# Kernel optimization log

Measured on AMD Instinct MI355X. Metric: run time of the kernel, lower is better.

The kernel has to match this reference:

```python
import jax, jax.numpy as jnp
import numpy as np

B, T, C, H = 4, 2048, 1024, 16
HD = C // H  # head dim = 64


def setup_inputs() -> dict:
    key = jax.random.key(0)
    k1, k2, k3, k4, k5 = jax.random.split(key, 5)
    s_in = 1.0 / np.sqrt(C)
    return {
        "x": jax.random.normal(k1, (B, T, C), dtype=jnp.float32),
        "W_attn": jax.random.uniform(k2, (C, 3 * C), dtype=jnp.float32, minval=-s_in, maxval=s_in),
        "b_attn": jax.random.uniform(k3, (3 * C,), dtype=jnp.float32, minval=-s_in, maxval=s_in),
        "W_proj": jax.random.uniform(k4, (C, C), dtype=jnp.float32, minval=-s_in, maxval=s_in),
        "b_proj": jax.random.uniform(k5, (C,), dtype=jnp.float32, minval=-s_in, maxval=s_in),
    }


def reference(x, W_attn, b_attn, W_proj, b_proj):
    Bx, Tx, Cx = x.shape
    qkv = x @ W_attn + b_attn                      # [B,T,3C]
    q, k, v = jnp.split(qkv, 3, axis=2)
    # [B,T,C] -> [B,H,T,HD]
    def heads(t):
        return t.reshape(Bx, Tx, H, HD).transpose(0, 2, 1, 3)
    q, k, v = heads(q), heads(k), heads(v)
    scale = 1.0 / np.sqrt(HD).astype(np.float32)
    att = jnp.einsum('bhqd,bhkd->bhqk', q, k) * scale
    causal = jnp.tril(jnp.ones((Tx, Tx), dtype=bool))
    att = jnp.where(causal[None, None], att, -jnp.inf)
    att = jax.nn.softmax(att, axis=-1)
    y = jnp.einsum('bhqk,bhkd->bhqd', att, v)      # [B,H,T,HD]
    y = y.transpose(0, 2, 1, 3).reshape(Bx, Tx, Cx)
    return y @ W_proj + b_proj
```

## Files before the change

kernel.cpp:

```cpp
#include <hip/hip_runtime.h>
#include <math.h>

#define Bn 4
#define Tn 2048
#define Cn 1024
#define Hn 16
#define HDn 64
#define Mn (Bn * Tn)

typedef unsigned short u16;
typedef unsigned int u32;
typedef __attribute__((ext_vector_type(8))) short bf16x8;
typedef __attribute__((ext_vector_type(8))) unsigned short us8;
typedef __attribute__((ext_vector_type(4))) float f32x4;
typedef __attribute__((ext_vector_type(16))) float f32x16;
typedef __attribute__((ext_vector_type(4))) unsigned int u32x4;

__device__ __forceinline__ float b2f(u16 u) {
    return __uint_as_float(((u32)u) << 16);
}
__device__ __forceinline__ u16 f2b(float f) {
    u32 u = __float_as_uint(f);
    return (u16)((u + 0x7FFFu + ((u >> 16) & 1u)) >> 16);
}
__device__ __forceinline__ u32 cvtpk(float a, float b) {
    u32 d;
    asm("v_cvt_pk_bf16_f32 %0, %1, %2" : "=v"(d) : "v"(a), "v"(b));
    return d;
}
__device__ __forceinline__ void pswap(u32& a, u32& b) {
    asm("v_permlane32_swap_b32 %0, %1" : "+v"(a), "+v"(b));
}
__device__ __forceinline__ float max3f(float a, float b, float c) {
    float d;
    asm("v_max3_f32 %0, %1, %2, %3" : "=v"(d) : "v"(a), "v"(b), "v"(c));
    return d;
}
#define EXP2R(x) __builtin_amdgcn_exp2f(x)

__device__ __forceinline__ int xcd_work(int bid, int nwg) {
    return (bid & 7) * (nwg >> 3) + (bid >> 3);
}

#define GLL(srcp, dstp)                                                     \
    __builtin_amdgcn_global_load_lds(                                       \
        (const __attribute__((address_space(1))) u32*)(srcp),               \
        (__attribute__((address_space(3))) u32*)(dstp), 16, 0, 0)

#define WAITCNT6() asm volatile("s_waitcnt vmcnt(6)" ::: "memory")
#define WAITCNT4() asm volatile("s_waitcnt vmcnt(4)" ::: "memory")
#define WAITCNT0() asm volatile("s_waitcnt vmcnt(0)" ::: "memory")

__global__ __launch_bounds__(256) void cvt_f32_bf16_kernel(
    const float4* __restrict__ in, ushort4* __restrict__ out, int n4)
{
    for (int i = blockIdx.x * 256 + threadIdx.x; i < n4; i += gridDim.x * 256) {
        float4 v = in[i];
        ushort4 o;
        o.x = f2b(v.x); o.y = f2b(v.y); o.z = f2b(v.z); o.w = f2b(v.w);
        out[i] = o;
    }
}

__global__ __launch_bounds__(256) void transpose_cvt_kernel(
    const float* __restrict__ in, u16* __restrict__ out, int R, int Cc)
{
    __shared__ u16 t[32][33];
    const int c0 = blockIdx.x * 32, r0 = blockIdx.y * 32;
    const int tx = threadIdx.x & 31, ty = threadIdx.x >> 5;
    #pragma unroll
    for (int i = 0; i < 32; i += 8)
        t[ty + i][tx] = f2b(in[(size_t)(r0 + ty + i) * Cc + c0 + tx]);
    __syncthreads();
    #pragma unroll
    for (int i = 0; i < 32; i += 8)
        out[(size_t)(c0 + ty + i) * R + r0 + tx] = t[tx][ty + i];
}

__global__ __launch_bounds__(256, 2) void gemm_qkv_kernel(
    const u16* __restrict__ A, const u16* __restrict__ BT,
    const float* __restrict__ bias,
    u16* __restrict__ outb, u16* __restrict__ vTout,
    int N, int K, int nx)
{
    __shared__ u16 Al[3][128 * 32];
    __shared__ u16 Bl[3][256 * 32];

    const int tid = threadIdx.x;
    const int workid = xcd_work(blockIdx.x, gridDim.x);
    const int brow = (workid / nx) * 128;
    const int bcol = (workid % nx) * 256;
    const int w  = tid >> 6;
    const int wr = w >> 1, wc = w & 1;
    const int l  = tid & 63;
    const int lr = l & 15;
    const int lk = (l >> 4) << 3;

    const int sr = l >> 2;
    const int sc = (l & 3) << 3;

    f32x4 acc[4][8];
    #pragma unroll
    for (int m = 0; m < 4; ++m)
        #pragma unroll
        for (int n = 0; n < 8; ++n) acc[m][n] = (f32x4){0.f, 0.f, 0.f, 0.f};

    #define STAGE_G(k0, bufi)                                                   \
        do {                                                                    \
            GLL(&A [(size_t)(brow + 32 * w +      sr) * K + (k0) + sc],         \
                &Al[bufi][(32 * w) * 32]);                                      \
            GLL(&A [(size_t)(brow + 32 * w + 16 + sr) * K + (k0) + sc],         \
                &Al[bufi][(32 * w + 16) * 32]);                                 \
            GLL(&BT[(size_t)(bcol + 64 * w +      sr) * K + (k0) + sc],         \
                &Bl[bufi][(64 * w) * 32]);                                      \
            GLL(&BT[(size_t)(bcol + 64 * w + 16 + sr) * K + (k0) + sc],         \
                &Bl[bufi][(64 * w + 16) * 32]);                                 \
            GLL(&BT[(size_t)(bcol + 64 * w + 32 + sr) * K + (k0) + sc],         \
                &Bl[bufi][(64 * w + 32) * 32]);                                 \
            GLL(&BT[(size_t)(bcol + 64 * w + 48 + sr) * K + (k0) + sc],         \
                &Bl[bufi][(64 * w + 48) * 32]);                                 \
        } while (0)

    const int T = K >> 5;
    STAGE_G(0, 0);
    STAGE_G(32, 1);

    int cur = 0;
    for (int t = 0; t < T; ++t) {
        if (t < T - 1) WAITCNT6();
        else           WAITCNT0();
        __builtin_amdgcn_s_barrier();

        if (t + 2 < T) {
            const int nb = cur + 2 >= 3 ? cur - 1 : cur + 2;
            STAGE_G((t + 2) << 5, nb);
        }

        bf16x8 a[4], b[8];
        #pragma unroll
        for (int m = 0; m < 4; ++m)
            a[m] = *(const bf16x8*)&Al[cur][(wr * 64 + m * 16 + lr) * 32 + lk];
        #pragma unroll
        for (int n = 0; n < 8; ++n)
            b[n] = *(const bf16x8*)&Bl[cur][(wc * 128 + n * 16 + lr) * 32 + lk];

        __builtin_amdgcn_s_setprio(1);
        #pragma unroll
        for (int m = 0; m < 4; ++m)
            #pragma unroll
            for (int n = 0; n < 8; ++n)
                acc[m][n] = __builtin_amdgcn_mfma_f32_16x16x32_bf16(
                    a[m], b[n], acc[m][n], 0, 0, 0);
        __builtin_amdgcn_s_setprio(0);

        cur = cur == 2 ? 0 : cur + 1;
    }
    #undef STAGE_G

    const int orow0 = brow + wr * 64 + ((l >> 4) << 2);
    const int ocol0 = bcol + wc * 128 + lr;
    if (bcol >= 2048) {
        #pragma unroll
        for (int n = 0; n < 8; ++n) {
            const int c = ocol0 + n * 16 - 2048;
            const float bv = bias[ocol0 + n * 16];
            #pragma unroll
            for (int m = 0; m < 4; ++m) {
                const int row0 = orow0 + m * 16;
                const int bb = row0 >> 11, t0 = row0 & 2047;
                ushort4 pk;
                pk.x = f2b(acc[m][n][0] + bv);
                pk.y = f2b(acc[m][n][1] + bv);
                pk.z = f2b(acc[m][n][2] + bv);
                pk.w = f2b(acc[m][n][3] + bv);
                *(ushort4*)&vTout[((size_t)bb * Cn + c) * Tn + t0] = pk;
            }
        }
    } else {
        #pragma unroll
        for (int n = 0; n < 8; ++n) {
            const int col = ocol0 + n * 16;
            const float bv = bias[col];
            #pragma unroll
            for (int m = 0; m < 4; ++m) {
                #pragma unroll
                for (int r = 0; r < 4; ++r) {
                    const int row = orow0 + m * 16 + r;
                    outb[(size_t)row * N + col] = f2b(acc[m][n][r] + bv);
                }
            }
        }
    }
}

__global__ __launch_bounds__(256) void gemm_proj_kernel(
    const u16* __restrict__ A, const u16* __restrict__ BT,
    const float* __restrict__ bias, float* __restrict__ outf,
    int N, int K, int nx)
{
    __shared__ u16 Al[3][128 * 32];
    __shared__ u16 Bl[3][128 * 32];

    const int tid = threadIdx.x;
    const int workid = xcd_work(blockIdx.x, gridDim.x);
    const int brow = (workid / nx) * 128;
    const int bcol = (workid % nx) * 128;
    const int w  = tid >> 6;
    const int wr = w >> 1, wc = w & 1;
    const int l  = tid & 63;
    const int lr = l & 15;
    const int lk = (l >> 4) << 3;

    const int r0s = tid >> 2,            c0s = (tid & 3) << 3;
    const int r1s = (256 + tid) >> 2;
    const int d0s = (tid & 192) * 8;
    const int d1s = (256 + (tid & 192)) * 8;

    f32x4 acc[4][4];
    #pragma unroll
    for (int m = 0; m < 4; ++m)
        #pragma unroll
        for (int n = 0; n < 4; ++n) acc[m][n] = (f32x4){0.f, 0.f, 0.f, 0.f};

    #define STAGE_P(k0, bufi)                                                \
        do {                                                                 \
            GLL(&A [(size_t)(brow + r0s) * K + (k0) + c0s], &Al[bufi][d0s]); \
            GLL(&BT[(size_t)(bcol + r0s) * K + (k0) + c0s], &Bl[bufi][d0s]); \
            GLL(&A [(size_t)(brow + r1s) * K + (k0) + c0s], &Al[bufi][d1s]); \
            GLL(&BT[(size_t)(bcol + r1s) * K + (k0) + c0s], &Bl[bufi][d1s]); \
        } while (0)

    const int T = K >> 5;
    STAGE_P(0, 0);
    STAGE_P(32, 1);

    int cur = 0;
    for (int t = 0; t < T; ++t) {
        if (t < T - 1) WAITCNT4();
        else           WAITCNT0();
        __builtin_amdgcn_s_barrier();

        if (t + 2 < T) {
            const int nb = cur + 2 >= 3 ? cur - 1 : cur + 2;
            STAGE_P((t + 2) << 5, nb);
        }

        bf16x8 a[4], b[4];
        #pragma unroll
        for (int m = 0; m < 4; ++m)
            a[m] = *(const bf16x8*)&Al[cur][(wr * 64 + m * 16 + lr) * 32 + lk];
        #pragma unroll
        for (int n = 0; n < 4; ++n)
            b[n] = *(const bf16x8*)&Bl[cur][(wc * 64 + n * 16 + lr) * 32 + lk];

        __builtin_amdgcn_s_setprio(1);
        #pragma unroll
        for (int m = 0; m < 4; ++m)
            #pragma unroll
            for (int n = 0; n < 4; ++n)
                acc[m][n] = __builtin_amdgcn_mfma_f32_16x16x32_bf16(
                    a[m], b[n], acc[m][n], 0, 0, 0);
        __builtin_amdgcn_s_setprio(0);

        cur = cur == 2 ? 0 : cur + 1;
    }
    #undef STAGE_P

    const int orow0 = brow + wr * 64 + ((l >> 4) << 2);
    const int ocol0 = bcol + wc * 64 + lr;
    #pragma unroll
    for (int n = 0; n < 4; ++n) {
        const int col = ocol0 + n * 16;
        const float bv = bias[col];
        #pragma unroll
        for (int m = 0; m < 4; ++m) {
            #pragma unroll
            for (int r = 0; r < 4; ++r) {
                const int row = orow0 + m * 16 + r;
                outf[(size_t)row * N + col] = acc[m][n][r] + bv;
            }
        }
    }
}

__global__ __launch_bounds__(256, 2) void attn_mfma8_kernel(
    const u16* __restrict__ qkvb, const u16* __restrict__ vT,
    u16* __restrict__ yb)
{
    __shared__ u16 Kb[3][64 * 64];
    __shared__ u16 Vb[3][64 * 64];

    const int tid = threadIdx.x;
    const int w   = tid >> 6;
    const int l   = tid & 63;
    const int q31 = l & 31;
    const int hi  = l >> 5;
    const int work = xcd_work(blockIdx.x, 512);
    const int pr  = work & 7;
    const int bh  = work >> 3;
    const int b   = bh >> 4, h = bh & 15;

    const float S2 = 0.18033688f;

    const u16* Kg = qkvb + (size_t)(b * Tn) * (3 * Cn) + Cn + h * HDn;
    const u16* Vg = vT + (size_t)bh * HDn * Tn;

    const int srow = l >> 3;
    const int schk = ((l & 7) ^ srow) << 3;
    const int rloc = w * 16;
    const int rsw8 = q31 & 7;

    #define STAGE_A(kt, bufi)                                                  \
        do {                                                                   \
            _Pragma("unroll")                                                  \
            for (int jc = 0; jc < 2; ++jc) {                                   \
                const int rr = rloc + jc * 8;                                  \
                GLL(Kg + (size_t)((kt) * 64 + rr + srow) * (3 * Cn) + schk,    \
                    &Kb[bufi][rr * 64]);                                       \
                GLL(Vg + (size_t)(rr + srow) * Tn + (kt) * 64 + schk,          \
                    &Vb[bufi][rr * 64]);                                       \
            }                                                                  \
        } while (0)

    #pragma unroll 1
    for (int half = 0; half < 2; ++half) {
        const int qt = half ? (15 - pr) : pr;
        const int ktmax = 2 * qt + 2;
        const int qrow0 = qt * 128 + w * 32;
        const int qglob = qrow0 + q31;

        const u16* Qp = qkvb + (size_t)(b * Tn + qglob) * (3 * Cn)
                        + h * HDn + hi * 8;
        bf16x8 qf[4];
        #pragma unroll
        for (int c = 0; c < 4; ++c) qf[c] = *(const bf16x8*)(Qp + c * 16);

        f32x16 O0, O1;
        #pragma unroll
        for (int r = 0; r < 16; ++r) { O0[r] = 0.f; O1[r] = 0.f; }
        float m = -INFINITY, ls = 0.f;

        STAGE_A(0, 0);
        STAGE_A(1, 1);

        int cur = 0;
        for (int kt = 0; kt < ktmax; ++kt) {
            if (kt < ktmax - 1) WAITCNT4();
            else                WAITCNT0();
            __builtin_amdgcn_s_barrier();

            if (kt + 2 < ktmax) {
                const int nb = cur + 2 >= 3 ? cur - 1 : cur + 2;
                STAGE_A(kt + 2, nb);
            }
            const u16* Kc = Kb[cur];
            const u16* Vc = Vb[cur];

            if (kt * 64 <= qrow0 + 31) {
                f32x16 S0, S1;
                #pragma unroll
                for (int r = 0; r < 16; ++r) { S0[r] = 0.f; S1[r] = 0.f; }
                __builtin_amdgcn_s_setprio(1);
                #pragma unroll
                for (int c = 0; c < 4; ++c) {
                    const int co = ((2 * c + hi) ^ rsw8) << 3;
                    const bf16x8 k0 = *(const bf16x8*)&Kc[q31 * 64 + co];
                    const bf16x8 k1 = *(const bf16x8*)&Kc[(32 + q31) * 64 + co];
                    S0 = __builtin_amdgcn_mfma_f32_32x32x16_bf16(k0, qf[c], S0, 0, 0, 0);
                    S1 = __builtin_amdgcn_mfma_f32_32x32x16_bf16(k1, qf[c], S1, 0, 0, 0);
                }
                __builtin_amdgcn_s_setprio(0);

                if (kt * 64 + 63 > qrow0) {
                    #pragma unroll
                    for (int r = 0; r < 16; ++r) {
                        const int kl = kt * 64 + (r & 3) + 8 * (r >> 2) + 4 * hi;
                        if (kl > qglob)      S0[r] = -INFINITY;
                        if (kl + 32 > qglob) S1[r] = -INFINITY;
                    }
                }

                float a0 = max3f(S0[0],  S0[1],  S0[2]);
                float a1 = max3f(S0[3],  S0[4],  S0[5]);
                float a2 = max3f(S0[6],  S0[7],  S0[8]);
                float a3 = max3f(S0[9],  S0[10], S0[11]);
                float a4 = max3f(S0[12], S0[13], S0[14]);
                float a5 = max3f(S0[15], S1[0],  S1[1]);
                float a6 = max3f(S1[2],  S1[3],  S1[4]);
                float a7 = max3f(S1[5],  S1[6],  S1[7]);
                float a8 = max3f(S1[8],  S1[9],  S1[10]);
                float a9 = max3f(S1[11], S1[12], S1[13]);
                float aA = fmaxf(S1[14], S1[15]);
                float b0 = max3f(a0, a1, a2);
                float b1 = max3f(a3, a4, a5);
                float b2 = max3f(a6, a7, a8);
                float b3 = fmaxf(a9, aA);
                float mt = fmaxf(fmaxf(b0, b1), fmaxf(b2, b3));
                mt = fmaxf(mt, __shfl_xor(mt, 32));

                float lscale = 1.f;
                if (__any(mt > m + 64.f)) {
                    const float mn = fmaxf(m, mt);
                    const float alpha = EXP2R((m - mn) * S2);
                    m = mn; lscale = alpha;
                    #pragma unroll
                    for (int r = 0; r < 16; ++r) {
                        const int qloc = (r & 3) + 8 * (r >> 2) + 4 * hi;
                        const float ar = __shfl(alpha, qloc);
                        O0[r] *= ar; O1[r] *= ar;
                    }
                }

                const float nms2 = -m * S2;
                float lt0 = 0.f, lt1 = 0.f;
                u32 w0[8], w1[8];
                #pragma unroll
                for (int i = 0; i < 8; ++i) {
                    const float p0 = EXP2R(fmaf(S0[2 * i],     S2, nms2));
                    const float p1 = EXP2R(fmaf(S0[2 * i + 1], S2, nms2));
                    const float p2 = EXP2R(fmaf(S1[2 * i],     S2, nms2));
                    const float p3 = EXP2R(fmaf(S1[2 * i + 1], S2, nms2));
                    lt0 += (p0 + p1);
                    lt1 += (p2 + p3);
                    w0[i] = cvtpk(p0, p1);
                    w1[i] = cvtpk(p2, p3);
                }
                float lt = lt0 + lt1;
                lt += __shfl_xor(lt, 32);
                ls = ls * lscale + lt;

                __builtin_amdgcn_s_setprio(1);
                #pragma unroll
                for (int t2 = 0; t2 < 2; ++t2) {
                    #pragma unroll
                    for (int c1 = 0; c1 < 2; ++c1) {
                        u32 a0w = t2 ? w1[4 * c1 + 0] : w0[4 * c1 + 0];
                        u32 b0w = t2 ? w1[4 * c1 + 2] : w0[4 * c1 + 2];
                        u32 a1w = t2 ? w1[4 * c1 + 1] : w0[4 * c1 + 1];
                        u32 b1w = t2 ? w1[4 * c1 + 3] : w0[4 * c1 + 3];
                        pswap(a0w, b0w);
                        pswap(a1w, b1w);
                        u32x4 fr; fr.x = a0w; fr.y = a1w; fr.z = b0w; fr.w = b1w;
                        const bf16x8 pf = __builtin_bit_cast(bf16x8, fr);
                        const int c = t2 * 2 + c1;
                        const int co = ((2 * c + hi) ^ rsw8) << 3;
                        const bf16x8 v0 = *(const bf16x8*)&Vc[q31 * 64 + co];
                        const bf16x8 v1 = *(const bf16x8*)&Vc[(32 + q31) * 64 + co];
                        O0 = __builtin_amdgcn_mfma_f32_32x32x16_bf16(pf, v0, O0, 0, 0, 0);
                        O1 = __builtin_amdgcn_mfma_f32_32x32x16_bf16(pf, v1, O1, 0, 0, 0);
                    }
                }
                __builtin_amdgcn_s_setprio(0);
            }

            cur = cur == 2 ? 0 : cur + 1;
        }

        __builtin_amdgcn_s_barrier();

        #pragma unroll
        for (int r = 0; r < 16; ++r) {
            const int qloc = (r & 3) + 8 * (r >> 2) + 4 * hi;
            const float inv = __builtin_amdgcn_rcpf(__shfl(ls, qloc));
            u16* yp = yb + (size_t)(b * Tn + qrow0 + qloc) * Cn + h * HDn + q31;
            yp[0]  = f2b(O0[r] * inv);
            yp[32] = f2b(O1[r] * inv);
        }
    }
    #undef STAGE_A
}

extern "C" void kernel_launch(void* const* d_in, const int* in_sizes, int n_in,
                              void* d_out, int out_size, void* d_ws, size_t ws_size,
                              hipStream_t stream)
{
    const float* x      = (const float*)d_in[0];
    const float* W_attn = (const float*)d_in[1];
    const float* b_attn = (const float*)d_in[2];
    const float* W_proj = (const float*)d_in[3];
    const float* b_proj = (const float*)d_in[4];
    float* out = (float*)d_out;

    u16* xb   = (u16*)d_ws;
    u16* WaT  = xb   + (size_t)Mn * Cn;
    u16* WpT  = WaT  + (size_t)3 * Cn * Cn;
    u16* qkvb = WpT  + (size_t)Cn * Cn;
    u16* yb   = qkvb + (size_t)Mn * 3 * Cn;
    u16* vT   = yb   + (size_t)Mn * Cn;

    cvt_f32_bf16_kernel<<<2048, 256, 0, stream>>>(
        (const float4*)x, (ushort4*)xb, Mn * Cn / 4);

    transpose_cvt_kernel<<<dim3(3 * Cn / 32, Cn / 32), 256, 0, stream>>>(
        W_attn, WaT, Cn, 3 * Cn);
    transpose_cvt_kernel<<<dim3(Cn / 32, Cn / 32), 256, 0, stream>>>(
        W_proj, WpT, Cn, Cn);

    gemm_qkv_kernel<<<64 * 12, 256, 0, stream>>>(
        xb, WaT, b_attn, qkvb, vT, 3 * Cn, Cn, 12);

    attn_mfma8_kernel<<<512, 256, 0, stream>>>(qkvb, vT, yb);

    gemm_proj_kernel<<<8 * 64, 256, 0, stream>>>(
        yb, WpT, b_proj, out, Cn, Cn, 8);
}
```

Before: 178.7 us.

## Restructure QKV GEMM to 256x256 tiles with 8 waves and swizzled LDS

The QKV projection GEMM now uses 256x256 output tiles computed by 512 threads (8 waves in a 2x4 grid), where it used 128x256 tiles with 4 waves. Each k-step is split into two half-phases separated by barriers, with the A and B global-to-LDS loads interleaved between them. An XOR swizzle on the LDS chunk index is meant to reduce bank conflicts on fragment reads. The aim is more operand reuse per tile and better overlap of loads with MFMA work. The cost is higher LDS use, extra barriers per iteration, and only 384 workgroups, which may leave the GPU less evenly loaded.

```diff
diff --git a/kernel.cpp b/kernel.cpp
--- a/kernel.cpp
+++ b/kernel.cpp
@@ -47,9 +47,9 @@
         (const __attribute__((address_space(1))) u32*)(srcp),               \
         (__attribute__((address_space(3))) u32*)(dstp), 16, 0, 0)
 
-#define WAITCNT6() asm volatile("s_waitcnt vmcnt(6)" ::: "memory")
 #define WAITCNT4() asm volatile("s_waitcnt vmcnt(4)" ::: "memory")
 #define WAITCNT0() asm volatile("s_waitcnt vmcnt(0)" ::: "memory")
+#define SCHEDB()   __builtin_amdgcn_sched_barrier(0)
 
 __global__ __launch_bounds__(256) void cvt_f32_bf16_kernel(
     const float4* __restrict__ in, ushort4* __restrict__ out, int n4)
@@ -77,95 +77,114 @@
         out[(size_t)(c0 + ty + i) * R + r0 + tx] = t[tx][ty + i];
 }
 
-__global__ __launch_bounds__(256, 2) void gemm_qkv_kernel(
+__global__ __launch_bounds__(512, 2) void gemm_qkv8_kernel(
     const u16* __restrict__ A, const u16* __restrict__ BT,
     const float* __restrict__ bias,
     u16* __restrict__ outb, u16* __restrict__ vTout,
     int N, int K, int nx)
 {
-    __shared__ u16 Al[3][128 * 32];
+    __shared__ u16 Al[3][256 * 32];
     __shared__ u16 Bl[3][256 * 32];
 
     const int tid = threadIdx.x;
     const int workid = xcd_work(blockIdx.x, gridDim.x);
-    const int brow = (workid / nx) * 128;
+    const int brow = (workid / nx) * 256;
     const int bcol = (workid % nx) * 256;
     const int w  = tid >> 6;
-    const int wr = w >> 1, wc = w & 1;
+    const int wm = w >> 2, wn = w & 3;
     const int l  = tid & 63;
     const int lr = l & 15;
-    const int lk = (l >> 4) << 3;
-
-    const int sr = l >> 2;
-    const int sc = (l & 3) << 3;
-
-    f32x4 acc[4][8];
+    const int g  = l >> 4;
+    const int rk = ((g ^ ((lr >> 1) & 3)) << 3);
+
+    const int srow = l >> 2;
+    const int schk = ((l & 3) ^ ((l >> 3) & 3)) << 3;
+
+    f32x4 acc[8][4];
     #pragma unroll
-    for (int m = 0; m < 4; ++m)
-        #pragma unroll
-        for (int n = 0; n < 8; ++n) acc[m][n] = (f32x4){0.f, 0.f, 0.f, 0.f};
-
-    #define STAGE_G(k0, bufi)                                                   \
-        do {                                                                    \
-            GLL(&A [(size_t)(brow + 32 * w +      sr) * K + (k0) + sc],         \
-                &Al[bufi][(32 * w) * 32]);                                      \
-            GLL(&A [(size_t)(brow + 32 * w + 16 + sr) * K + (k0) + sc],         \
-                &Al[bufi][(32 * w + 16) * 32]);                                 \
-            GLL(&BT[(size_t)(bcol + 64 * w +      sr) * K + (k0) + sc],         \
-                &Bl[bufi][(64 * w) * 32]);                                      \
-            GLL(&BT[(size_t)(bcol + 64 * w + 16 + sr) * K + (k0) + sc],         \
-                &Bl[bufi][(64 * w + 16) * 32]);                                 \
-            GLL(&BT[(size_t)(bcol + 64 * w + 32 + sr) * K + (k0) + sc],         \
-                &Bl[bufi][(64 * w + 32) * 32]);                                 \
-            GLL(&BT[(size_t)(bcol + 64 * w + 48 + sr) * K + (k0) + sc],         \
-                &Bl[bufi][(64 * w + 48) * 32]);                                 \
+    for (int m = 0; m < 8; ++m)
+        #pragma unroll
+        for (int n = 0; n < 4; ++n) acc[m][n] = (f32x4){0.f, 0.f, 0.f, 0.f};
+
+    #define STG_A(k0, bufi)                                                    \
+        do {                                                                   \
+            GLL(&A[(size_t)(brow +       w * 16 + srow) * K + (k0) + schk],    \
+                &Al[bufi][(w * 16) * 32]);                                     \
+            GLL(&A[(size_t)(brow + 128 + w * 16 + srow) * K + (k0) + schk],    \
+                &Al[bufi][(128 + w * 16) * 32]);                               \
         } while (0)
+    #define STG_B(k0, bufi)                                                    \
+        do {                                                                   \
+            GLL(&BT[(size_t)(bcol +       w * 16 + srow) * K + (k0) + schk],   \
+                &Bl[bufi][(w * 16) * 32]);                                     \
+            GLL(&BT[(size_t)(bcol + 128 + w * 16 + srow) * K + (k0) + schk],   \
+                &Bl[bufi][(128 + w * 16) * 32]);                               \
+        } while (0)
 
     const int T = K >> 5;
-    STAGE_G(0, 0);
-    STAGE_G(32, 1);
-
-    int cur = 0;
+    STG_A(0, 0);  STG_B(0, 0);
+    STG_A(32, 1); STG_B(32, 1);
+
     for (int t = 0; t < T; ++t) {
-        if (t < T - 1) WAITCNT6();
+        const int cur = t % 3;
+        const int nxt = (t + 2) % 3;
+        const int k0n = (t + 2) << 5;
+        const u16* Ac = Al[cur];
+        const u16* Bc = Bl[cur];
+
+        if (t < T - 1) WAITCNT4();
         else           WAITCNT0();
         __builtin_amdgcn_s_barrier();
-
-        if (t + 2 < T) {
-            const int nb = cur + 2 >= 3 ? cur - 1 : cur + 2;
-            STAGE_G((t + 2) << 5, nb);
-        }
-
-        bf16x8 a[4], b[8];
+        SCHEDB();
+        if (t + 2 < T) STG_A(k0n, nxt);
+
+        bf16x8 bfr[4], afr[4];
+        #pragma unroll
+        for (int n = 0; n < 4; ++n)
+            bfr[n] = *(const bf16x8*)&Bc[(wn * 64 + n * 16 + lr) * 32 + rk];
         #pragma unroll
         for (int m = 0; m < 4; ++m)
-            a[m] = *(const bf16x8*)&Al[cur][(wr * 64 + m * 16 + lr) * 32 + lk];
-        #pragma unroll
-        for (int n = 0; n < 8; ++n)
-            b[n] = *(const bf16x8*)&Bl[cur][(wc * 128 + n * 16 + lr) * 32 + lk];
+            afr[m] = *(const bf16x8*)&Ac[(wm * 128 + m * 16 + lr) * 32 + rk];
 
         __builtin_amdgcn_s_setprio(1);
         #pragma unroll
         for (int m = 0; m < 4; ++m)
             #pragma unroll
-            for (int n = 0; n < 8; ++n)
+            for (int n = 0; n < 4; ++n)
                 acc[m][n] = __builtin_amdgcn_mfma_f32_16x16x32_bf16(
-                    a[m], b[n], acc[m][n], 0, 0, 0);
+                    afr[m], bfr[n], acc[m][n], 0, 0, 0);
         __builtin_amdgcn_s_setprio(0);
-
-        cur = cur == 2 ? 0 : cur + 1;
+        __builtin_amdgcn_s_barrier();
+        SCHEDB();
+
+        if (t + 2 < T) STG_B(k0n, nxt);
+        #pragma unroll
+        for (int m = 0; m < 4; ++m)
+            afr[m] = *(const bf16x8*)&Ac[(wm * 128 + 64 + m * 16 + lr) * 32 + rk];
+
+        __builtin_amdgcn_s_setprio(1);
+        #pragma unroll
+        for (int m = 0; m < 4; ++m)
+            #pragma unroll
+            for (int n = 0; n < 4; ++n)
+                acc[4 + m][n] = __builtin_amdgcn_mfma_f32_16x16x32_bf16(
+                    afr[m], bfr[n], acc[4 + m][n], 0, 0, 0);
+        __builtin_amdgcn_s_setprio(0);
+        __builtin_amdgcn_s_barrier();
+        SCHEDB();
     }
-    #undef STAGE_G
-
-    const int orow0 = brow + wr * 64 + ((l >> 4) << 2);
-    const int ocol0 = bcol + wc * 128 + lr;
+    #undef STG_A
+    #undef STG_B
+
+    const int orow0 = brow + wm * 128 + (g << 2);
+    const int ocol0 = bcol + wn * 64 + lr;
     if (bcol >= 2048) {
         #pragma unroll
-        for (int n = 0; n < 8; ++n) {
+        for (int n = 0; n < 4; ++n) {
             const int c = ocol0 + n * 16 - 2048;
             const float bv = bias[ocol0 + n * 16];
             #pragma unroll
-            for (int m = 0; m < 4; ++m) {
+            for (int m = 0; m < 8; ++m) {
                 const int row0 = orow0 + m * 16;
                 const int bb = row0 >> 11, t0 = row0 & 2047;
                 ushort4 pk;
@@ -178,11 +197,11 @@
         }
     } else {
         #pragma unroll
-        for (int n = 0; n < 8; ++n) {
+        for (int n = 0; n < 4; ++n) {
             const int col = ocol0 + n * 16;
             const float bv = bias[col];
             #pragma unroll
-            for (int m = 0; m < 4; ++m) {
+            for (int m = 0; m < 8; ++m) {
                 #pragma unroll
                 for (int r = 0; r < 4; ++r) {
                     const int row = orow0 + m * 16 + r;
@@ -496,7 +515,7 @@
     transpose_cvt_kernel<<<dim3(Cn / 32, Cn / 32), 256, 0, stream>>>(
         W_proj, WpT, Cn, Cn);
 
-    gemm_qkv_kernel<<<64 * 12, 256, 0, stream>>>(
+    gemm_qkv8_kernel<<<32 * 12, 512, 0, stream>>>(
         xb, WaT, b_attn, qkvb, vT, 3 * Cn, Cn, 12);
 
     attn_mfma8_kernel<<<512, 256, 0, stream>>>(qkvb, vT, yb);
```

New measurement: 200.0 us. +11.9%, slower.
